# Kernel optimization log

Measured on AMD Instinct MI355X. Metric: run time of the kernel, lower is better.

The kernel has to match this reference:

```python
import jax, jax.numpy as jnp
import numpy as np

C = 2048  # per-input channels; concat channels = 2*C = 4096
B, H, W = 2, 64, 64


def setup_inputs() -> dict:
    key = jax.random.key(0)
    ks = jax.random.split(key, 8)
    s = 0.02
    return {
        "f_rgb": jax.random.normal(ks[0], (B, C, H, W), jnp.float32),
        "f_i": jax.random.normal(ks[1], (B, C, H, W), jnp.float32),
        "wq": jax.random.normal(ks[2], (C, 2 * C), jnp.float32) * s,
        "bq": jnp.zeros((C,), jnp.float32),
        "wk": jax.random.normal(ks[3], (C, 2 * C), jnp.float32) * s,
        "bk": jnp.zeros((C,), jnp.float32),
        "wv": jax.random.normal(ks[4], (2 * C, 2 * C), jnp.float32) * s,
        "bv": jnp.zeros((2 * C,), jnp.float32),
    }


def reference(f_rgb, f_i, wq, bq, wk, bk, wv, bv):
    b, c, h, w = f_rgb.shape
    n = h * w
    # concat along channels: [B, 2C, N]
    x = jnp.concatenate([f_rgb, f_i], axis=1).reshape(b, 2 * c, n)
    # 1x1 convs == per-pixel matmuls over channels
    Q = jnp.einsum('oc,bcn->bon', wq, x) + bq[None, :, None]  # [B, C, N]
    K = jnp.einsum('oc,bcn->bon', wk, x) + bk[None, :, None]  # [B, C, N]
    V = jnp.einsum('oc,bcn->bon', wv, x) + bv[None, :, None]  # [B, 2C, N]
    scale = jnp.sqrt(jnp.asarray(2 * c, jnp.float32))  # sqrt(channels of concat)
    attn = jax.nn.softmax(jnp.einsum('bcn,bcm->bnm', Q, K) / scale, axis=-1)  # [B, N, N]
    # out[b,c,n] = sum_m V[b,c,m] * attn[b,n,m]  (bmm(V, attn^T))
    out = jnp.einsum('bcm,bnm->bcn', V, attn).reshape(b, 2 * c, h, w)
    f_final = out[:, :c] + out[:, c:]
    return (f_final, f_rgb, f_i, attn)
```

## Files before the change

kernel.cpp:

```cpp
#include <hip/hip_runtime.h>
#include <hip/hip_bf16.h>


#define B_   2
#define C_   2048
#define N_   4096
#define C2_  4096

#define LDSB 131072

typedef __hip_bfloat16 bf16_t;
typedef __bf16 bf16x8 __attribute__((ext_vector_type(8)));
typedef float floatx4 __attribute__((ext_vector_type(4)));

__device__ inline void load_lds16(const void* g, void* l) {
  __builtin_amdgcn_global_load_lds(
      (const __attribute__((address_space(1))) void*)g,
      (__attribute__((address_space(3))) void*)l, 16, 0, 0);
}

__device__ inline unsigned short f2bf(float f) {
  return __builtin_bit_cast(unsigned short, __float2bfloat16(f));
}

__device__ inline void cstore(float* p, float v)  { *p = v; }
__device__ inline void cstore(bf16_t* p, float v) { *p = __float2bfloat16(v); }

template <typename OutT>
__global__ __launch_bounds__(512, 2) void gemm_bt8(
    const bf16_t* __restrict__ A, const bf16_t* __restrict__ Bt,
    OutT* __restrict__ Cm, int K, int lda, int ldb, int ldc,
    long long abst, long long bbst, long long cbst,
    const float* __restrict__ bias_m, const float* __restrict__ bias_n,
    float scale)
{
  extern __shared__ char smem[];

  const int tid  = threadIdx.x;
  const int lane = tid & 63;
  const int wave = tid >> 6;
  const int wm   = wave >> 2;
  const int wn   = wave & 3;
  const int fr   = lane & 15;
  const int kc   = lane >> 4;

  const int gx  = gridDim.x, gy = gridDim.y;
  const int nxy = gx * gy;
  const int nwg = nxy * gridDim.z;
  int wg = blockIdx.x + gx * (blockIdx.y + gy * blockIdx.z);
  wg = (wg & 7) * (nwg >> 3) + (wg >> 3);
  const int bz  = wg / nxy;
  const int rxy = wg - bz * nxy;
  const int by  = rxy / gx;
  const int bx  = rxy - by * gx;

  const long long bM = (long long)by * 256;
  const long long bN = (long long)bx * 256;

  const bf16_t* Ab = A  + (long long)bz * abst;
  const bf16_t* Bb = Bt + (long long)bz * bbst;
  OutT*         Cb = Cm + (long long)bz * cbst;

  const int srow = lane >> 3;
  const int scol = 8 * ((lane & 7) ^ srow);
  const bf16_t* gA = Ab + (bM + wave * 8 + srow) * (long long)lda + scol;
  const bf16_t* gB = Bb + (bN + wave * 8 + srow) * (long long)ldb + scol;
  char* sbase = smem + wave * 1024;

  auto stage = [&](int p, int ab, int h, int kt) {
    const long long ld = ab ? ldb : lda;
    const bf16_t* g = (ab ? gB : gA) + (long long)h * 128 * ld
                                     + (long long)kt * 64;
    char* l = sbase + p * 65536 + ab * 32768 + h * 16384;
    load_lds16(g,            l);
    load_lds16(g + 64 * ld,  l + 8192);
  };

  floatx4 acc[8][4];
#pragma unroll
  for (int i = 0; i < 8; i++)
#pragma unroll
    for (int j = 0; j < 4; j++) acc[i][j] = (floatx4){0.f, 0.f, 0.f, 0.f};

  bf16x8 af[4][2];
  bf16x8 bfr[4][2];

  auto readAh = [&](int p, int mh) {
#pragma unroll
    for (int i = 0; i < 4; i++) {
      const int row = (mh * 4 + i) * 32 + wm * 16 + fr;
      const char* rb = smem + p * 65536 + row * 128;
#pragma unroll
      for (int ks = 0; ks < 2; ks++)
        af[i][ks] = *(const bf16x8*)(rb +
            (((ks * 64) + kc * 16) ^ ((fr & 7) << 4)));
    }
  };
  auto readBh = [&](int p, int nh) {
#pragma unroll
    for (int j = 0; j < 2; j++) {
      const int row = (nh * 2 + j) * 64 + wn * 16 + fr;
      const char* rb = smem + p * 65536 + 32768 + row * 128;
#pragma unroll
      for (int ks = 0; ks < 2; ks++)
        bfr[nh * 2 + j][ks] = *(const bf16x8*)(rb +
            (((ks * 64) + kc * 16) ^ ((fr & 7) << 4)));
    }
  };
  auto quad = [&](int mh, int nh) {
    __builtin_amdgcn_s_setprio(1);
#pragma unroll
    for (int ks = 0; ks < 2; ks++)
#pragma unroll
      for (int i = 0; i < 4; i++)
#pragma unroll
        for (int j = 0; j < 2; j++)
          acc[mh * 4 + i][nh * 2 + j] = __builtin_amdgcn_mfma_f32_16x16x32_bf16(
              af[i][ks], bfr[nh * 2 + j][ks], acc[mh * 4 + i][nh * 2 + j],
              0, 0, 0);
    __builtin_amdgcn_s_setprio(0);
  };

  const int NT = K >> 6;

  {
    const int t1 = (NT > 1) ? 1 : 0;
    stage(0, 0, 0, 0); stage(0, 1, 0, 0);
    stage(0, 0, 1, 0); stage(0, 1, 1, 0);
    stage(1, 0, 0, t1); stage(1, 1, 0, t1);
    stage(1, 0, 1, t1);
  }
  asm volatile("s_waitcnt vmcnt(6)" ::: "memory");
  __builtin_amdgcn_s_barrier();

  for (int t = 0; t < NT; ++t) {
    const int p  = t & 1, q = p ^ 1;
    const int t1 = (t + 1 < NT) ? t + 1 : NT - 1;
    const int t2 = (t + 2 < NT) ? t + 2 : NT - 1;

    readAh(p, 0); readBh(p, 0);
    stage(q, 1, 1, t1);
    __builtin_amdgcn_s_barrier();
    quad(0, 0);
    __builtin_amdgcn_s_barrier();

    readBh(p, 1);
    stage(p, 0, 0, t2);
    __builtin_amdgcn_s_barrier();
    quad(0, 1);
    __builtin_amdgcn_s_barrier();

    readAh(p, 1);
    stage(p, 1, 0, t2);
    __builtin_amdgcn_s_barrier();
    quad(1, 1);
    __builtin_amdgcn_s_barrier();

    stage(p, 0, 1, t2);
    __builtin_amdgcn_s_barrier();
    quad(1, 0);
    asm volatile("s_waitcnt vmcnt(6)" ::: "memory");
    __builtin_amdgcn_s_barrier();
  }

  const int rown = (lane >> 4) * 4;
#pragma unroll
  for (int mi = 0; mi < 8; mi++) {
#pragma unroll
    for (int ni = 0; ni < 4; ni++) {
      const long long n = bN + ni * 64 + wn * 16 + fr;
      const float bnv = bias_n ? bias_n[n] : 0.f;
#pragma unroll
      for (int r = 0; r < 4; r++) {
        const long long m = bM + mi * 32 + wm * 16 + rown + r;
        const float bmv = bias_m ? bias_m[m] : 0.f;
        cstore(&Cb[m * (long long)ldc + n], acc[mi][ni][r] * scale + bnv + bmv);
      }
    }
  }
}

__global__ __launch_bounds__(256) void pack_xt(
    const float* __restrict__ f_rgb, const float* __restrict__ f_i,
    float* __restrict__ out_rgb, float* __restrict__ out_i,
    bf16_t* __restrict__ xt)
{
  const int b  = blockIdx.z >> 1;
  const int wh = blockIdx.z & 1;
  const float* src = (wh ? f_i : f_rgb) + (long long)b * C_ * N_;
  float*       pt  = (wh ? out_i : out_rgb) + (long long)b * C_ * N_;
  const int c0 = blockIdx.y * 64, n0 = blockIdx.x * 64;
  __shared__ float tile[64][65];

  const int tid = threadIdx.x;
  {
    const int tn = tid & 63, tc4 = tid >> 6;
#pragma unroll
    for (int r = 0; r < 16; r++) {
      const int c = tc4 * 16 + r;
      const long long idx = (long long)(c0 + c) * N_ + n0 + tn;
      const float v = src[idx];
      pt[idx] = v;
      tile[tn][c] = v;
    }
  }
  __syncthreads();
  {
    const int tc = tid & 63, tn4 = tid >> 6;
#pragma unroll
    for (int r = 0; r < 16; r++) {
      const int n = tn4 * 16 + r;
      xt[((long long)b * N_ + n0 + n) * C2_ + wh * C_ + c0 + tc] =
          __float2bfloat16(tile[n][tc]);
    }
  }
}

__global__ __launch_bounds__(256) void conv_wqk(
    const float* __restrict__ wq, const float* __restrict__ wk,
    unsigned short* __restrict__ dst)
{
  const long long i = ((long long)blockIdx.x * 256 + threadIdx.x) * 4;
  const int o = (int)(i >> 12);
  const long long c = i & 4095;
  const float* src = (o < C_) ? (wq + (long long)o * C2_ + c)
                              : (wk + (long long)(o - C_) * C2_ + c);
  const float4 f = *(const float4*)src;
  *(ushort4*)(dst + i) = make_ushort4(f2bf(f.x), f2bf(f.y), f2bf(f.z), f2bf(f.w));
}

__global__ __launch_bounds__(256) void conv_wvsum(
    const float* __restrict__ wv, unsigned short* __restrict__ dst)
{
  const long long i = ((long long)blockIdx.x * 256 + threadIdx.x) * 4;
  const float4 a = *(const float4*)(wv + i);
  const float4 b = *(const float4*)(wv + i + (long long)C_ * C2_);
  *(ushort4*)(dst + i) = make_ushort4(f2bf(a.x + b.x), f2bf(a.y + b.y),
                                      f2bf(a.z + b.z), f2bf(a.w + b.w));
}

__global__ __launch_bounds__(256) void conv_bias(
    const float* __restrict__ bq, const float* __restrict__ bk,
    const float* __restrict__ bv, float* __restrict__ bqk,
    float* __restrict__ bvsum)
{
  const int i = blockIdx.x * 256 + threadIdx.x;
  bqk[i] = (i < C_) ? bq[i] : bk[i - C_];
  if (i < C_) bvsum[i] = bv[i] + bv[i + C_];
}

__global__ __launch_bounds__(256) void softmax_rows(
    float* __restrict__ attn, bf16_t* __restrict__ attn_bf)
{
  const long long row = blockIdx.x;
  float4*  p4  = (float4*)(attn + row * N_);
  ushort4* pb4 = (ushort4*)(attn_bf + row * N_);
  const int tid = threadIdx.x;
  const int lane = tid & 63, wave = tid >> 6;

  float4 v[4];
  float mx = -3.4e38f;
#pragma unroll
  for (int i = 0; i < 4; i++) {
    v[i] = p4[tid + i * 256];
    mx = fmaxf(mx, fmaxf(fmaxf(v[i].x, v[i].y), fmaxf(v[i].z, v[i].w)));
  }
#pragma unroll
  for (int off = 32; off >= 1; off >>= 1) mx = fmaxf(mx, __shfl_xor(mx, off, 64));

  __shared__ float redm[4];
  __shared__ float reds[4];
  if (lane == 0) redm[wave] = mx;
  __syncthreads();
  mx = fmaxf(fmaxf(redm[0], redm[1]), fmaxf(redm[2], redm[3]));

  float s = 0.f;
#pragma unroll
  for (int i = 0; i < 4; i++) {
    v[i].x = __expf(v[i].x - mx); v[i].y = __expf(v[i].y - mx);
    v[i].z = __expf(v[i].z - mx); v[i].w = __expf(v[i].w - mx);
    s += (v[i].x + v[i].y) + (v[i].z + v[i].w);
  }
#pragma unroll
  for (int off = 32; off >= 1; off >>= 1) s += __shfl_xor(s, off, 64);
  if (lane == 0) reds[wave] = s;
  __syncthreads();
  s = reds[0] + reds[1] + reds[2] + reds[3];
  const float inv = 1.f / s;
#pragma unroll
  for (int i = 0; i < 4; i++) {
    float4 a;
    a.x = v[i].x * inv; a.y = v[i].y * inv;
    a.z = v[i].z * inv; a.w = v[i].w * inv;
    p4[tid + i * 256]  = a;
    pb4[tid + i * 256] = make_ushort4(f2bf(a.x), f2bf(a.y), f2bf(a.z), f2bf(a.w));
  }
}

extern "C" void kernel_launch(void* const* d_in, const int* in_sizes, int n_in,
                              void* d_out, int out_size, void* d_ws, size_t ws_size,
                              hipStream_t stream) {
  const float* f_rgb = (const float*)d_in[0];
  const float* f_i   = (const float*)d_in[1];
  const float* wq    = (const float*)d_in[2];
  const float* bq    = (const float*)d_in[3];
  const float* wk    = (const float*)d_in[4];
  const float* bk    = (const float*)d_in[5];
  const float* wv    = (const float*)d_in[6];
  const float* bv    = (const float*)d_in[7];

  float* out       = (float*)d_out;
  float* out_ff    = out;
  float* out_rgb   = out + (size_t)B_ * C_ * N_;
  float* out_fi    = out_rgb + (size_t)B_ * C_ * N_;
  float* out_attn  = out_fi + (size_t)B_ * C_ * N_;

  char* ws = (char*)d_ws;
  size_t off = 0;
  auto alloc = [&](size_t bytes) {
    size_t o = off; off += (bytes + 255) & ~(size_t)255; return o;
  };
  bf16_t* xt   = (bf16_t*)(ws + alloc((size_t)B_ * N_ * C2_ * 2));
  bf16_t* wqk  = (bf16_t*)(ws + alloc((size_t)C2_ * C2_ * 2));
  bf16_t* wvs  = (bf16_t*)(ws + alloc((size_t)C_ * C2_ * 2));
  bf16_t* qkt  = (bf16_t*)(ws + alloc((size_t)B_ * N_ * C2_ * 2));
  bf16_t* vsum = (bf16_t*)(ws + alloc((size_t)B_ * C_ * N_ * 2));
  bf16_t* abf  = (bf16_t*)(ws + alloc((size_t)B_ * N_ * N_ * 2));
  float*  bqk  = (float*)(ws + alloc((size_t)C2_ * 4));
  float*  bvs  = (float*)(ws + alloc((size_t)C_ * 4));
  (void)ws_size; (void)in_sizes; (void)n_in; (void)out_size;

  static bool attr_done = false;
  if (!attr_done) {
    (void)hipFuncSetAttribute((const void*)&gemm_bt8<bf16_t>,
        hipFuncAttributeMaxDynamicSharedMemorySize, LDSB);
    (void)hipFuncSetAttribute((const void*)&gemm_bt8<float>,
        hipFuncAttributeMaxDynamicSharedMemorySize, LDSB);
    attr_done = true;
  }

  const dim3 blk(256);
  const dim3 blk8(512);

  pack_xt<<<dim3(N_ / 64, C_ / 64, B_ * 2), blk, 0, stream>>>(
      f_rgb, f_i, out_rgb, out_fi, xt);
  conv_wqk<<<dim3((C2_ * C2_) / (4 * 256)), blk, 0, stream>>>(
      wq, wk, (unsigned short*)wqk);
  conv_wvsum<<<dim3((C_ * C2_) / (4 * 256)), blk, 0, stream>>>(
      wv, (unsigned short*)wvs);
  conv_bias<<<dim3(C2_ / 256), blk, 0, stream>>>(bq, bk, bv, bqk, bvs);

  const long long sNN = (long long)N_ * C2_;
  const long long sCN = (long long)C_ * N_;

  gemm_bt8<bf16_t><<<dim3(C2_ / 256, N_ / 256, B_), blk8, LDSB, stream>>>(
      xt, wqk, qkt, C2_, C2_, C2_, C2_, sNN, 0, sNN, nullptr, bqk, 1.0f);

  gemm_bt8<bf16_t><<<dim3(N_ / 256, C_ / 256, B_), blk8, LDSB, stream>>>(
      wvs, xt, vsum, C2_, C2_, C2_, N_, 0, sNN, sCN, bvs, nullptr, 1.0f);

  gemm_bt8<float><<<dim3(N_ / 256, N_ / 256, B_), blk8, LDSB, stream>>>(
      qkt, qkt + C_, out_attn, C_, C2_, C2_, N_, sNN, sNN, sNN,
      nullptr, nullptr, 1.0f / 64.0f);

  softmax_rows<<<dim3(B_ * N_), blk, 0, stream>>>(out_attn, abf);

  gemm_bt8<float><<<dim3(N_ / 256, C_ / 256, B_), blk8, LDSB, stream>>>(
      vsum, abf, out_ff, N_, N_, N_, N_, sCN, sNN, sCN,
      nullptr, nullptr, 1.0f);
}
```

Before: 1.147 ms.

## Restructure GEMM main loop to two-phase schedule and vectorize transpose stores

```diff
diff --git a/kernel.cpp b/kernel.cpp
--- a/kernel.cpp
+++ b/kernel.cpp
@@ -125,43 +125,38 @@
 
   {
     const int t1 = (NT > 1) ? 1 : 0;
-    stage(0, 0, 0, 0); stage(0, 1, 0, 0);
-    stage(0, 0, 1, 0); stage(0, 1, 1, 0);
+    stage(0, 0, 0, 0);  stage(0, 1, 0, 0);
+    stage(0, 0, 1, 0);  stage(0, 1, 1, 0);
     stage(1, 0, 0, t1); stage(1, 1, 0, t1);
-    stage(1, 0, 1, t1);
-  }
-  asm volatile("s_waitcnt vmcnt(6)" ::: "memory");
+    stage(1, 0, 1, t1); stage(1, 1, 1, t1);
+  }
+  asm volatile("s_waitcnt vmcnt(8)" ::: "memory");
   __builtin_amdgcn_s_barrier();
 
   for (int t = 0; t < NT; ++t) {
-    const int p  = t & 1, q = p ^ 1;
-    const int t1 = (t + 1 < NT) ? t + 1 : NT - 1;
+    const int p  = t & 1;
     const int t2 = (t + 2 < NT) ? t + 2 : NT - 1;
 
-    readAh(p, 0); readBh(p, 0);
-    stage(q, 1, 1, t1);
+    readAh(p, 0);
+    readBh(p, 0); readBh(p, 1);
+    quad(0, 0);
+    quad(0, 1);
+    readAh(p, 1);
+    asm volatile("s_waitcnt lgkmcnt(0)" ::: "memory");
     __builtin_amdgcn_s_barrier();
-    quad(0, 0);
+
+    stage(p, 0, 0, t2); stage(p, 1, 0, t2);
+    stage(p, 0, 1, t2); stage(p, 1, 1, t2);
+
+    quad(1, 1);
+    quad(1, 0);
+
+    __builtin_amdgcn_sched_barrier(0);
+    asm volatile("s_waitcnt vmcnt(8)" ::: "memory");
     __builtin_amdgcn_s_barrier();
-
-    readBh(p, 1);
-    stage(p, 0, 0, t2);
-    __builtin_amdgcn_s_barrier();
-    quad(0, 1);
-    __builtin_amdgcn_s_barrier();
-
-    readAh(p, 1);
-    stage(p, 1, 0, t2);
-    __builtin_amdgcn_s_barrier();
-    quad(1, 1);
-    __builtin_amdgcn_s_barrier();
-
-    stage(p, 0, 1, t2);
-    __builtin_amdgcn_s_barrier();
-    quad(1, 0);
-    asm volatile("s_waitcnt vmcnt(6)" ::: "memory");
-    __builtin_amdgcn_s_barrier();
-  }
+  }
+
+  asm volatile("s_waitcnt vmcnt(0)" ::: "memory");
 
   const int rown = (lane >> 4) * 4;
 #pragma unroll
@@ -206,12 +201,15 @@
   }
   __syncthreads();
   {
-    const int tc = tid & 63, tn4 = tid >> 6;
-#pragma unroll
-    for (int r = 0; r < 16; r++) {
-      const int n = tn4 * 16 + r;
-      xt[((long long)b * N_ + n0 + n) * C2_ + wh * C_ + c0 + tc] =
-          __float2bfloat16(tile[n][tc]);
+    const int tc4 = (tid & 15) * 4;
+    const int tnr = tid >> 4;
+#pragma unroll
+    for (int r = 0; r < 4; r++) {
+      const int n = r * 16 + tnr;
+      const ushort4 w = make_ushort4(
+          f2bf(tile[n][tc4]),     f2bf(tile[n][tc4 + 1]),
+          f2bf(tile[n][tc4 + 2]), f2bf(tile[n][tc4 + 3]));
+      *(ushort4*)&xt[((long long)b * N_ + n0 + n) * C2_ + wh * C_ + c0 + tc4] = w;
     }
   }
 }
```

Result: slower. 1.172 ms (+2.1%).
